# Kernel optimization log

Hardware: AMD Instinct MI355X
Metric: run time of the kernel (lower is better)

The kernel has to match this reference:

```python
import jax, jax.numpy as jnp
import numpy as np

D_MODEL, N_HEADS, D_K, D_FF, N_LAYERS, VOCAB, TGT_LEN = 512, 8, 64, 2048, 4, 32000, 1024
B, S_ENC = 4, 1024


def layernorm(x, g, b, eps=1e-6):
    mu = jnp.mean(x, axis=-1, keepdims=True)
    var = jnp.var(x, axis=-1, keepdims=True)
    return g * (x - mu) / jnp.sqrt(var + eps) + b


def sinusoid_pos_enc(seq_len, d_model):
    # source indexes positions 5 .. tgt_len+4 into the sinusoid table
    pos = jnp.arange(5, seq_len + 5, dtype=jnp.float32)[:, None]
    i = jnp.arange(d_model)
    angle = pos / jnp.power(10000.0, (2 * (i // 2)).astype(jnp.float32) / d_model)
    return jnp.where(i % 2 == 0, jnp.sin(angle), jnp.cos(angle))


def mha(xq, xkv, W, b, g, beta, mask):
    # W: [4, d, d] = (Wq, Wk, Wv, Wo); mask: [B,1,q,k], attend where mask != 0
    Bsz, Sq, _ = xq.shape
    q = (xq @ W[0] + b[0]).reshape(Bsz, Sq, N_HEADS, D_K).transpose(0, 2, 1, 3)
    k = (xkv @ W[1] + b[1]).reshape(Bsz, -1, N_HEADS, D_K).transpose(0, 2, 1, 3)
    v = (xkv @ W[2] + b[2]).reshape(Bsz, -1, N_HEADS, D_K).transpose(0, 2, 1, 3)
    scores = jnp.einsum('bhqd,bhkd->bhqk', q, k) / jnp.sqrt(jnp.float32(D_K))
    scores = jnp.where(mask == 0, jnp.float32(-1e9), scores)
    attn = jax.nn.softmax(scores, axis=-1)
    ctx = jnp.einsum('bhqk,bhkd->bhqd', attn, v).transpose(0, 2, 1, 3).reshape(Bsz, Sq, D_MODEL)
    out = ctx @ W[3] + b[3]
    return layernorm(out + xq, g, beta)


def setup_inputs() -> dict:
    key = jax.random.key(0)
    ks = jax.random.split(key, 8)
    sc = 0.02
    return {
        'dec_inputs': jax.random.randint(ks[0], (B, TGT_LEN), 0, VOCAB, dtype=jnp.int32),
        'enc_inputs': jax.random.randint(ks[1], (B, S_ENC), 0, 50, dtype=jnp.int32),
        'enc_outputs': jax.random.normal(ks[2], (B, S_ENC, D_MODEL), jnp.float32),
        'tgt_emb': jax.random.normal(ks[3], (VOCAB, D_MODEL), jnp.float32) * sc,
        'self_W': jax.random.normal(ks[4], (N_LAYERS, 4, D_MODEL, D_MODEL), jnp.float32) * sc,
        'self_b': jnp.zeros((N_LAYERS, 4, D_MODEL), jnp.float32),
        'enc_W': jax.random.normal(ks[5], (N_LAYERS, 4, D_MODEL, D_MODEL), jnp.float32) * sc,
        'enc_b': jnp.zeros((N_LAYERS, 4, D_MODEL), jnp.float32),
        'ffn_W1': jax.random.normal(ks[6], (N_LAYERS, D_MODEL, D_FF), jnp.float32) * sc,
        'ffn_b1': jnp.zeros((N_LAYERS, D_FF), jnp.float32),
        'ffn_W2': jax.random.normal(ks[7], (N_LAYERS, D_FF, D_MODEL), jnp.float32) * sc,
        'ffn_b2': jnp.zeros((N_LAYERS, D_MODEL), jnp.float32),
        'ln_g': jnp.ones((N_LAYERS, 3, D_MODEL), jnp.float32),
        'ln_b': jnp.zeros((N_LAYERS, 3, D_MODEL), jnp.float32),
    }


def reference(dec_inputs, enc_inputs, enc_outputs, tgt_emb, self_W, self_b, enc_W, enc_b,
              ffn_W1, ffn_b1, ffn_W2, ffn_b2, ln_g, ln_b):
    Bsz, S = dec_inputs.shape
    x = tgt_emb[dec_inputs] + sinusoid_pos_enc(S, D_MODEL)
    # self-attn mask: (pad_k OR lower-triangular) > 0, attend where nonzero (as in source)
    pad_self = (dec_inputs == 0).astype(jnp.float32)[:, None, None, :]      # [B,1,1,S]
    sub = jnp.tril(jnp.ones((S, S), jnp.float32))                           # [S,S]
    self_mask = ((pad_self + sub) > 0).astype(jnp.float32)                  # [B,1,S,S]
    # cross-attn mask: 1 where enc key is PAD; attend where nonzero (as in source)
    cross_mask = (enc_inputs == 0).astype(jnp.float32)[:, None, None, :]    # [B,1,1,S_enc]

    def step(h, p):
        sW, sb, eW, eb, W1, b1, W2, b2, g, bb = p
        h = mha(h, h, sW, sb, g[0], bb[0], self_mask)
        h = mha(h, enc_outputs, eW, eb, g[1], bb[1], cross_mask)
        f = jax.nn.relu(h @ W1 + b1) @ W2 + b2   # Conv1D(k=1) == pointwise dense
        h = layernorm(f + h, g[2], bb[2])
        return h, None

    x, _ = jax.lax.scan(step, x, (self_W, self_b, enc_W, enc_b,
                                  ffn_W1, ffn_b1, ffn_W2, ffn_b2, ln_g, ln_b))
    return x


if __name__ == '__main__':
    out = reference(**setup_inputs())
    print(out.shape, out.dtype)
```

## Files before the change

kernel.cpp:

```cpp
#include <hip/hip_runtime.h>
#include <math.h>

#define D_MODEL 512
#define N_HEADS 8
#define D_KH    64
#define D_FF    2048
#define N_LAYERS 4
#define BSZ     4
#define SEQ     1024

typedef __attribute__((ext_vector_type(8))) __bf16 bf16x8;
typedef __attribute__((ext_vector_type(8))) short  s16x8;
typedef __attribute__((ext_vector_type(4))) float  f32x4;

union BF8 { s16x8 s; bf16x8 b; };

static __device__ inline unsigned short f2b(float f) {
    unsigned u = __float_as_uint(f);
    unsigned r = (u + 0x7fffu + ((u >> 16) & 1u)) >> 16;
    return (unsigned short)r;
}

static __device__ __forceinline__ void async16(const unsigned short* g, unsigned short* l) {
    __builtin_amdgcn_global_load_lds((const __attribute__((address_space(1))) unsigned int*)g,
                                     (__attribute__((address_space(3))) unsigned int*)l, 16, 0, 0);
}

__global__ void embed_kernel(const int* __restrict__ dec, const float* __restrict__ emb,
                             float* __restrict__ x, unsigned short* __restrict__ xb) {
    int idx = blockIdx.x * blockDim.x + threadIdx.x;
    int d  = idx % D_MODEL;
    int bs = idx / D_MODEL;
    int s  = bs % SEQ;
    int tok = dec[bs];
    float pos = (float)(s + 5);
    float e = (float)(d & ~1) * (1.0f / (float)D_MODEL);
    float ang = pos * __expf(-9.210340372f * e);
    float pe = (d & 1) ? __cosf(ang) : __sinf(ang);
    float v = emb[(size_t)tok * D_MODEL + d] + pe;
    x[idx] = v;
    xb[idx] = f2b(v);
}

__global__ void cvt_bf16_kernel(const float* __restrict__ in, unsigned short* __restrict__ outp, int n4) {
    int i = blockIdx.x * blockDim.x + threadIdx.x;
    if (i < n4) {
        float4 f = ((const float4*)in)[i];
        ushort4 h;
        h.x = f2b(f.x); h.y = f2b(f.y); h.z = f2b(f.z); h.w = f2b(f.w);
        ((ushort4*)outp)[i] = h;
    }
}

__global__ void wt_all_kernel(const float* __restrict__ selfW, const float* __restrict__ encW,
                              const float* __restrict__ W1, const float* __restrict__ W2,
                              unsigned short* __restrict__ wtS, unsigned short* __restrict__ wtE,
                              unsigned short* __restrict__ wtF1, unsigned short* __restrict__ wtF2) {
    __shared__ unsigned short Tb[64][72];
    int tile = blockIdx.x;
    int which = tile >> 10, rem = tile & 1023;
    const float* src; unsigned short* dst; int K, N, z, kt, ntile;
    if (which <= 1) {
        src = which ? encW : selfW; dst = which ? wtE : wtS;
        K = 512; N = 512;
        z = rem >> 6; int r2 = rem & 63; kt = r2 & 7; ntile = r2 >> 3;
    } else if (which == 2) {
        src = W1; dst = wtF1; K = 512; N = 2048;
        z = rem >> 8; int r2 = rem & 255; kt = r2 & 7; ntile = r2 >> 3;
    } else {
        src = W2; dst = wtF2; K = 2048; N = 512;
        z = rem >> 8; int r2 = rem & 255; kt = r2 >> 3; ntile = r2 & 7;
    }
    int k0 = kt * 64, n0 = ntile * 64;
    size_t zoff = (size_t)z * K * N;
    src += zoff; dst += zoff;
    int t = threadIdx.x;
    int kr = t & 63, sg = t >> 6;
    const float* sp = src + (size_t)(k0 + kr) * N + n0 + sg * 16;
    #pragma unroll
    for (int j = 0; j < 4; j++) {
        float4 f = *(const float4*)(sp + 4 * j);
        Tb[sg * 16 + 4 * j + 0][kr] = f2b(f.x);
        Tb[sg * 16 + 4 * j + 1][kr] = f2b(f.y);
        Tb[sg * 16 + 4 * j + 2][kr] = f2b(f.z);
        Tb[sg * 16 + 4 * j + 3][kr] = f2b(f.w);
    }
    __syncthreads();
    unsigned short* dp = dst + (size_t)(n0 + kr) * K + k0 + sg * 16;
    *(s16x8*)(dp)     = *(const s16x8*)&Tb[kr][sg * 16];
    *(s16x8*)(dp + 8) = *(const s16x8*)&Tb[kr][sg * 16 + 8];
}

__global__ void prep_kernel(const int* __restrict__ dec, const int* __restrict__ enc,
                            int* __restrict__ cntEnc, int* __restrict__ listEnc,
                            int* __restrict__ anyPadDec) {
    int b = blockIdx.x;
    int lane = threadIdx.x;
    int base = 0;
    for (int c0 = 0; c0 < SEQ; c0 += 64) {
        bool z = (enc[b * SEQ + c0 + lane] == 0);
        unsigned long long mask = __ballot(z);
        int pre = __popcll(mask & ((1ull << lane) - 1ull));
        if (z) listEnc[b * SEQ + base + pre] = c0 + lane;
        base += __popcll(mask);
    }
    if (lane == 0) cntEnc[b] = base;
    for (int c0 = 0; c0 < SEQ; c0 += 64) {
        bool z = (dec[b * SEQ + c0 + lane] == 0);
        unsigned long long mask = __ballot(z);
        if (lane == 0) anyPadDec[b * (SEQ / 64) + (c0 >> 6)] = (mask != 0ull) ? 1 : 0;
    }
}

template<int OUTBF16, int RELU, int QKV>
__launch_bounds__(256, 3)
__global__ void gemm_lds_kernel(const unsigned short* __restrict__ A, const unsigned short* __restrict__ A1,
                                const unsigned short* __restrict__ Wt, const float* __restrict__ bias,
                                void* __restrict__ C_, void* __restrict__ C1, void* __restrict__ C2,
                                int M, int N, int K) {
    __shared__ unsigned short lds[2][12288];
    int m0 = blockIdx.x * 128, n0;
    if (QKV) {
        int j = blockIdx.y >> 3;
        n0 = (int)(blockIdx.y & 7) * 64;
        Wt += (size_t)j * (D_MODEL * D_MODEL);
        bias += j * D_MODEL;
        if (j) A = A1;
        if (j == 1) C_ = C1; else if (j == 2) C_ = C2;
    } else n0 = blockIdx.y * 64;

    int t = threadIdx.x, w = t >> 6, lane = t & 63;
    int g = lane >> 4, c = lane & 15;
    int l3 = lane >> 3, l7 = lane & 7;
    int srcoff = 8 * (l7 ^ l3);

    const unsigned short* Abase = A  + (size_t)m0 * K;
    const unsigned short* Bbase = Wt + (size_t)n0 * K;

    f32x4 acc[2][4];
    #pragma unroll
    for (int mi = 0; mi < 2; mi++)
        #pragma unroll
        for (int nj = 0; nj < 4; nj++) acc[mi][nj] = (f32x4){0.f, 0.f, 0.f, 0.f};

#define STAGE(BUF, KT) do {                                                         \
        unsigned short* Lb_ = &lds[BUF][0];                                         \
        int k0_ = (KT) * 64;                                                        \
        _Pragma("unroll")                                                           \
        for (int i_ = 0; i_ < 4; i_++) {                                            \
            int q_ = w * 4 + i_;                                                    \
            async16(Abase + (size_t)(q_ * 8 + l3) * K + k0_ + srcoff, Lb_ + q_ * 512); \
        }                                                                           \
        _Pragma("unroll")                                                           \
        for (int i_ = 0; i_ < 2; i_++) {                                            \
            int q_ = w * 2 + i_;                                                    \
            async16(Bbase + (size_t)(q_ * 8 + l3) * K + k0_ + srcoff, Lb_ + 8192 + q_ * 512); \
        }                                                                           \
    } while (0)

    int nt = K >> 6;
    STAGE(0, 0);
    __syncthreads();
    for (int kt = 0; kt < nt; kt++) {
        int cur = kt & 1;
        if (kt + 1 < nt) STAGE(cur ^ 1, kt + 1);
        const unsigned short* Lb = &lds[cur][0];
        BF8 a[2][2], b[2][4];
        #pragma unroll
        for (int kk = 0; kk < 2; kk++) {
            int xo = (kk * 32 + g * 8) ^ ((c & 7) * 8);
            #pragma unroll
            for (int mi = 0; mi < 2; mi++)
                a[kk][mi].s = *(const s16x8*)&Lb[(w * 32 + mi * 16 + c) * 64 + xo];
            #pragma unroll
            for (int nj = 0; nj < 4; nj++)
                b[kk][nj].s = *(const s16x8*)&Lb[8192 + (nj * 16 + c) * 64 + xo];
        }
        #pragma unroll
        for (int kk = 0; kk < 2; kk++)
            #pragma unroll
            for (int mi = 0; mi < 2; mi++)
                #pragma unroll
                for (int nj = 0; nj < 4; nj++)
                    acc[mi][nj] = __builtin_amdgcn_mfma_f32_16x16x32_bf16(a[kk][mi].b, b[kk][nj].b, acc[mi][nj], 0, 0, 0);
        __syncthreads();
    }
#undef STAGE

    #pragma unroll
    for (int mi = 0; mi < 2; mi++) {
        #pragma unroll
        for (int nj = 0; nj < 4; nj++) {
            #pragma unroll
            for (int r = 0; r < 4; r++) {
                int row = m0 + w * 32 + mi * 16 + g * 4 + r;
                int col = n0 + nj * 16 + c;
                float v = acc[mi][nj][r] + bias[col];
                if (RELU) v = fmaxf(v, 0.0f);
                if (OUTBF16) ((unsigned short*)C_)[(size_t)row * N + col] = f2b(v);
                else         ((float*)C_)[(size_t)row * N + col] = v;
            }
        }
    }
}

template<int OUTBF16, int RELU>
__launch_bounds__(256, 4)
__global__ void gemm64_kernel(const unsigned short* __restrict__ A,
                              const unsigned short* __restrict__ Wt, const float* __restrict__ bias,
                              void* __restrict__ C_, int M, int N, int K) {
    __shared__ unsigned short lds[2][8192];
    int m0 = blockIdx.x * 64, n0 = blockIdx.y * 64;

    int t = threadIdx.x, w = t >> 6, lane = t & 63;
    int wm = w >> 1, wn = w & 1;
    int g = lane >> 4, c = lane & 15;
    int l3 = lane >> 3, l7 = lane & 7;
    int srcoff = 8 * (l7 ^ l3);

    const unsigned short* Abase = A  + (size_t)m0 * K;
    const unsigned short* Bbase = Wt + (size_t)n0 * K;

    f32x4 acc[2][2];
    #pragma unroll
    for (int mi = 0; mi < 2; mi++)
        #pragma unroll
        for (int nj = 0; nj < 2; nj++) acc[mi][nj] = (f32x4){0.f, 0.f, 0.f, 0.f};

#define STAGE64(BUF, KT) do {                                                       \
        unsigned short* Lb_ = &lds[BUF][0];                                         \
        int k0_ = (KT) * 64;                                                        \
        _Pragma("unroll")                                                           \
        for (int i_ = 0; i_ < 2; i_++) {                                            \
            int q_ = w * 2 + i_;                                                    \
            async16(Abase + (size_t)(q_ * 8 + l3) * K + k0_ + srcoff, Lb_ + q_ * 512); \
            async16(Bbase + (size_t)(q_ * 8 + l3) * K + k0_ + srcoff, Lb_ + 4096 + q_ * 512); \
        }                                                                           \
    } while (0)

    int nt = K >> 6;
    STAGE64(0, 0);
    __syncthreads();
    for (int kt = 0; kt < nt; kt++) {
        int cur = kt & 1;
        if (kt + 1 < nt) STAGE64(cur ^ 1, kt + 1);
        const unsigned short* Lb = &lds[cur][0];
        BF8 a[2][2], b[2][2];
        #pragma unroll
        for (int kk = 0; kk < 2; kk++) {
            int xo = (kk * 32 + g * 8) ^ ((c & 7) * 8);
            #pragma unroll
            for (int mi = 0; mi < 2; mi++)
                a[kk][mi].s = *(const s16x8*)&Lb[(wm * 32 + mi * 16 + c) * 64 + xo];
            #pragma unroll
            for (int nj = 0; nj < 2; nj++)
                b[kk][nj].s = *(const s16x8*)&Lb[4096 + (wn * 32 + nj * 16 + c) * 64 + xo];
        }
        #pragma unroll
        for (int kk = 0; kk < 2; kk++)
            #pragma unroll
            for (int mi = 0; mi < 2; mi++)
                #pragma unroll
                for (int nj = 0; nj < 2; nj++)
                    acc[mi][nj] = __builtin_amdgcn_mfma_f32_16x16x32_bf16(a[kk][mi].b, b[kk][nj].b, acc[mi][nj], 0, 0, 0);
        __syncthreads();
    }
#undef STAGE64

    #pragma unroll
    for (int mi = 0; mi < 2; mi++) {
        #pragma unroll
        for (int nj = 0; nj < 2; nj++) {
            #pragma unroll
            for (int r = 0; r < 4; r++) {
                int row = m0 + wm * 32 + mi * 16 + g * 4 + r;
                int col = n0 + wn * 32 + nj * 16 + c;
                float v = acc[mi][nj][r] + bias[col];
                if (RELU) v = fmaxf(v, 0.0f);
                if (OUTBF16) ((unsigned short*)C_)[(size_t)row * N + col] = f2b(v);
                else         ((float*)C_)[(size_t)row * N + col] = v;
            }
        }
    }
}

template<int OUTBF16, int RELU>
__launch_bounds__(256, 2)
__global__ void gemm128_kernel(const unsigned short* __restrict__ A,
                               const unsigned short* __restrict__ Wt, const float* __restrict__ bias,
                               void* __restrict__ C_, int M, int N, int K) {
    __shared__ unsigned short lds[2][16384];
    int m0 = blockIdx.x * 128, n0 = blockIdx.y * 128;

    int t = threadIdx.x, w = t >> 6, lane = t & 63;
    int wm = w >> 1, wn = w & 1;
    int g = lane >> 4, c = lane & 15;
    int l3 = lane >> 3, l7 = lane & 7;
    int srcoff = 8 * (l7 ^ l3);

    const unsigned short* Abase = A  + (size_t)m0 * K;
    const unsigned short* Bbase = Wt + (size_t)n0 * K;

    f32x4 acc[4][4];
    #pragma unroll
    for (int mi = 0; mi < 4; mi++)
        #pragma unroll
        for (int nj = 0; nj < 4; nj++) acc[mi][nj] = (f32x4){0.f, 0.f, 0.f, 0.f};

#define STAGE128(BUF, KT) do {                                                      \
        unsigned short* Lb_ = &lds[BUF][0];                                         \
        int k0_ = (KT) * 64;                                                        \
        _Pragma("unroll")                                                           \
        for (int i_ = 0; i_ < 4; i_++) {                                            \
            int q_ = w * 4 + i_;                                                    \
            async16(Abase + (size_t)(q_ * 8 + l3) * K + k0_ + srcoff, Lb_ + q_ * 512); \
            async16(Bbase + (size_t)(q_ * 8 + l3) * K + k0_ + srcoff, Lb_ + 8192 + q_ * 512); \
        }                                                                           \
    } while (0)

    int nt = K >> 6;
    STAGE128(0, 0);
    __syncthreads();
    for (int kt = 0; kt < nt; kt++) {
        int cur = kt & 1;
        if (kt + 1 < nt) STAGE128(cur ^ 1, kt + 1);
        const unsigned short* Lb = &lds[cur][0];
        BF8 a[2][4], b[2][4];
        #pragma unroll
        for (int kk = 0; kk < 2; kk++) {
            int xo = (kk * 32 + g * 8) ^ ((c & 7) * 8);
            #pragma unroll
            for (int mi = 0; mi < 4; mi++)
                a[kk][mi].s = *(const s16x8*)&Lb[(wm * 64 + mi * 16 + c) * 64 + xo];
            #pragma unroll
            for (int nj = 0; nj < 4; nj++)
                b[kk][nj].s = *(const s16x8*)&Lb[8192 + (wn * 64 + nj * 16 + c) * 64 + xo];
        }
        #pragma unroll
        for (int kk = 0; kk < 2; kk++)
            #pragma unroll
            for (int mi = 0; mi < 4; mi++)
                #pragma unroll
                for (int nj = 0; nj < 4; nj++)
                    acc[mi][nj] = __builtin_amdgcn_mfma_f32_16x16x32_bf16(a[kk][mi].b, b[kk][nj].b, acc[mi][nj], 0, 0, 0);
        __syncthreads();
    }
#undef STAGE128

    #pragma unroll
    for (int mi = 0; mi < 4; mi++) {
        #pragma unroll
        for (int nj = 0; nj < 4; nj++) {
            #pragma unroll
            for (int r = 0; r < 4; r++) {
                int row = m0 + wm * 64 + mi * 16 + g * 4 + r;
                int col = n0 + wn * 64 + nj * 16 + c;
                float v = acc[mi][nj][r] + bias[col];
                if (RELU) v = fmaxf(v, 0.0f);
                if (OUTBF16) ((unsigned short*)C_)[(size_t)row * N + col] = f2b(v);
                else         ((float*)C_)[(size_t)row * N + col] = v;
            }
        }
    }
}

#define RS 72
template<int MODE>
__global__ void attn_kernel(const unsigned short* __restrict__ Q, const unsigned short* __restrict__ K,
                            const unsigned short* __restrict__ V, const int* __restrict__ ids,
                            const int* __restrict__ list, const int* __restrict__ cnt,
                            const int* __restrict__ anyPad,
                            unsigned short* __restrict__ O_, int Sq, int Sk) {
    __shared__ unsigned short Kl[2][64][RS];
    __shared__ unsigned short Vt[2][64][RS];
    __shared__ unsigned short Ps[4][16][RS];
    __shared__ short act[16];
    __shared__ int nActS;

    int blk = blockIdx.x;
    int qt, bh;
    if (MODE) {
        int hi = blk >> 8, pair = blk & 255;
        bh = pair >> 3;
        int qtp = pair & 7;
        qt = hi ? (15 - qtp) : qtp;
    } else {
        qt = blk & 15;
        bh = blk >> 4;
    }
    int h = bh % N_HEADS;
    int b = bh / N_HEADS;
    int qbase = qt * 64;
    int t = threadIdx.x;
    int w = t >> 6, lane = t & 63;
    int g = lane >> 4, c = lane & 15;

    BF8 qf[2];
    {
        int qrow = qbase + w * 16 + c;
        const unsigned short* qp = Q + ((size_t)(b * Sq + qrow)) * D_MODEL + h * D_KH;
        qf[0].s = *(const s16x8*)(qp + 8 * g);
        qf[1].s = *(const s16x8*)(qp + 8 * g + 32);
    }

    int nk = 0;
    bool gathered = false;
    if (!MODE) {
        nk = cnt[b];
        gathered = (nk > 0);
    }

    if (t == 0) {
        int n = 0;
        if (MODE) {
            for (int kt2 = 0; kt2 < (Sk >> 6); kt2++)
                if (kt2 <= qt || anyPad[b * (Sk >> 6) + kt2]) act[n++] = (short)kt2;
        } else {
            int tt = gathered ? ((nk + 63) >> 6) : (Sk >> 6);
            for (int kt2 = 0; kt2 < tt; kt2++) act[n++] = (short)kt2;
        }
        nActS = n;
    }
    __syncthreads();
    int nAct = nActS;

    float m[4], l[4];
    f32x4 Oacc[4];
    #pragma unroll
    for (int r = 0; r < 4; r++) { m[r] = -INFINITY; l[r] = 0.0f; }
    #pragma unroll
    for (int ds = 0; ds < 4; ds++) Oacc[ds] = (f32x4){0.f, 0.f, 0.f, 0.f};

    s16x8 kreg0, kreg1, vreg0, vreg1;
    int kr0 = t >> 3,        ks0 = t & 7;
    int kr1 = (t + 256) >> 3, ks1 = (t + 256) & 7;

#define LOADT(KT) do {                                                                \
        int k0_ = (KT) * 64;                                                          \
        int krow0 = k0_ + kr0, krow1 = k0_ + kr1;                                     \
        if (gathered) {                                                               \
            krow0 = list[b * Sk + (krow0 < nk ? krow0 : nk - 1)];                     \
            krow1 = list[b * Sk + (krow1 < nk ? krow1 : nk - 1)];                     \
        }                                                                             \
        kreg0 = *(const s16x8*)(K + ((size_t)(b * Sk + krow0)) * D_MODEL + h * D_KH + ks0 * 8); \
        kreg1 = *(const s16x8*)(K + ((size_t)(b * Sk + krow1)) * D_MODEL + h * D_KH + ks1 * 8); \
        int li = k0_ + lane, vrow = li;                                               \
        if (gathered) vrow = list[b * Sk + (li < nk ? li : nk - 1)];                  \
        const unsigned short* vp = V + ((size_t)(b * Sk + vrow)) * D_MODEL + h * D_KH + w * 16; \
        vreg0 = *(const s16x8*)(vp);                                                  \
        vreg1 = *(const s16x8*)(vp + 8);                                              \
    } while (0)

#define WRITET(BUF) do {                                                              \
        *(s16x8*)&Kl[BUF][kr0][ks0 * 8] = kreg0;                                      \
        *(s16x8*)&Kl[BUF][kr1][ks1 * 8] = kreg1;                                      \
        _Pragma("unroll")                                                             \
        for (int j = 0; j < 8; j++) Vt[BUF][w * 16 + j][lane] = ((unsigned short*)&vreg0)[j]; \
        _Pragma("unroll")                                                             \
        for (int j = 0; j < 8; j++) Vt[BUF][w * 16 + 8 + j][lane] = ((unsigned short*)&vreg1)[j]; \
    } while (0)

    LOADT(act[0]);
    WRITET(0);
    __syncthreads();
    for (int i = 0; i < nAct; i++) {
        int cur = i & 1;
        int k0 = (int)act[i] * 64;
        if (i + 1 < nAct) LOADT(act[i + 1]);

        f32x4 S[4];
        #pragma unroll
        for (int sub = 0; sub < 4; sub++) {
            BF8 b0, b1;
            b0.s = *(const s16x8*)&Kl[cur][sub * 16 + c][8 * g];
            b1.s = *(const s16x8*)&Kl[cur][sub * 16 + c][8 * g + 32];
            f32x4 s = (f32x4){0.f, 0.f, 0.f, 0.f};
            s = __builtin_amdgcn_mfma_f32_16x16x32_bf16(qf[0].b, b0.b, s, 0, 0, 0);
            s = __builtin_amdgcn_mfma_f32_16x16x32_bf16(qf[1].b, b1.b, s, 0, 0, 0);
            S[sub] = s;
        }

        #pragma unroll
        for (int sub = 0; sub < 4; sub++) {
            int k = k0 + sub * 16 + c;
            bool pad;
            if (MODE) pad = (ids[b * Sk + k] == 0);
            else      pad = gathered ? (k < nk) : false;
            #pragma unroll
            for (int r = 0; r < 4; r++) {
                bool att;
                if (MODE) {
                    int qrow = qbase + w * 16 + g * 4 + r;
                    att = pad || (k <= qrow);
                } else att = pad;
                S[sub][r] = att ? S[sub][r] * 0.125f : -1e9f;
            }
        }

        #pragma unroll
        for (int r = 0; r < 4; r++) {
            float mx = fmaxf(fmaxf(S[0][r], S[1][r]), fmaxf(S[2][r], S[3][r]));
            #pragma unroll
            for (int o = 8; o > 0; o >>= 1) mx = fmaxf(mx, __shfl_xor(mx, o));
            float mn = fmaxf(m[r], mx);
            float sc = __expf(m[r] - mn);
            float lsum = 0.f;
            #pragma unroll
            for (int sub = 0; sub < 4; sub++) {
                float p = __expf(S[sub][r] - mn);
                S[sub][r] = p;
                lsum += p;
            }
            #pragma unroll
            for (int o = 8; o > 0; o >>= 1) lsum += __shfl_xor(lsum, o);
            l[r] = l[r] * sc + lsum;
            m[r] = mn;
            #pragma unroll
            for (int ds = 0; ds < 4; ds++) Oacc[ds][r] *= sc;
        }

        #pragma unroll
        for (int sub = 0; sub < 4; sub++)
            #pragma unroll
            for (int r = 0; r < 4; r++)
                Ps[w][g * 4 + r][sub * 16 + c] = f2b(S[sub][r]);

        #pragma unroll
        for (int kk = 0; kk < 2; kk++) {
            BF8 pa;
            pa.s = *(const s16x8*)&Ps[w][c][8 * g + kk * 32];
            #pragma unroll
            for (int ds = 0; ds < 4; ds++) {
                BF8 vb;
                vb.s = *(const s16x8*)&Vt[cur][ds * 16 + c][8 * g + kk * 32];
                Oacc[ds] = __builtin_amdgcn_mfma_f32_16x16x32_bf16(pa.b, vb.b, Oacc[ds], 0, 0, 0);
            }
        }

        if (i + 1 < nAct) WRITET(cur ^ 1);
        __syncthreads();
    }
#undef LOADT
#undef WRITET

    #pragma unroll
    for (int r = 0; r < 4; r++) {
        float inv = 1.0f / l[r];
        int qrow = qbase + w * 16 + g * 4 + r;
        unsigned short* op = O_ + ((size_t)(b * Sq + qrow)) * D_MODEL + h * D_KH;
        #pragma unroll
        for (int ds = 0; ds < 4; ds++)
            op[ds * 16 + c] = f2b(Oacc[ds][r] * inv);
    }
}

template<int WRITEB>
__global__ void ln_residual_kernel(const float* __restrict__ f, const float* __restrict__ h,
                                   const float* __restrict__ g, const float* __restrict__ bb,
                                   float* __restrict__ out, unsigned short* __restrict__ outb) {
    int row  = blockIdx.x * 4 + threadIdx.x / 64;
    int lane = threadIdx.x % 64;
    const float* fr = f + (size_t)row * D_MODEL;
    const float* hr = h + (size_t)row * D_MODEL;
    float v[8];
    float s = 0.f;
    #pragma unroll
    for (int i = 0; i < 8; i++) {
        v[i] = fr[lane + i * 64] + hr[lane + i * 64];
        s += v[i];
    }
    #pragma unroll
    for (int o = 32; o > 0; o >>= 1) s += __shfl_xor(s, o);
    float mu = s * (1.0f / 512.0f);
    float ss = 0.f;
    #pragma unroll
    for (int i = 0; i < 8; i++) { float d = v[i] - mu; ss += d * d; }
    #pragma unroll
    for (int o = 32; o > 0; o >>= 1) ss += __shfl_xor(ss, o);
    float var = ss * (1.0f / 512.0f);
    float inv = 1.0f / sqrtf(var + 1e-6f);
    #pragma unroll
    for (int i = 0; i < 8; i++) {
        int d = lane + i * 64;
        float o2 = g[d] * (v[i] - mu) * inv + bb[d];
        out[(size_t)row * D_MODEL + d] = o2;
        if (WRITEB) outb[(size_t)row * D_MODEL + d] = f2b(o2);
    }
}

extern "C" void kernel_launch(void* const* d_in, const int* in_sizes, int n_in,
                              void* d_out, int out_size, void* d_ws, size_t ws_size,
                              hipStream_t stream) {
    const int*   dec     = (const int*)d_in[0];
    const int*   enc_ids = (const int*)d_in[1];
    const float* enc_out = (const float*)d_in[2];
    const float* emb     = (const float*)d_in[3];
    const float* self_W  = (const float*)d_in[4];
    const float* self_b  = (const float*)d_in[5];
    const float* enc_W   = (const float*)d_in[6];
    const float* enc_b   = (const float*)d_in[7];
    const float* W1      = (const float*)d_in[8];
    const float* b1      = (const float*)d_in[9];
    const float* W2      = (const float*)d_in[10];
    const float* b2      = (const float*)d_in[11];
    const float* ln_g    = (const float*)d_in[12];
    const float* ln_b    = (const float*)d_in[13];
    float* out = (float*)d_out;

    const size_t NTOK = (size_t)BSZ * SEQ;
    float* x  = (float*)d_ws;
    float* bA = x + NTOK * D_MODEL;
    unsigned short* xb   = (unsigned short*)(bA + NTOK * D_MODEL);
    unsigned short* encb = xb + NTOK * D_MODEL;
    unsigned short* bQ = encb + NTOK * D_MODEL;
    unsigned short* bK = bQ + NTOK * D_MODEL;
    unsigned short* bV = bK + NTOK * D_MODEL;
    unsigned short* bD = bV + NTOK * D_MODEL;
    unsigned short* bH = bQ;
    unsigned short* wtS  = bD + NTOK * D_MODEL;
    unsigned short* wtE  = wtS + (size_t)N_LAYERS * 4 * D_MODEL * D_MODEL;
    unsigned short* wtF1 = wtE + (size_t)N_LAYERS * 4 * D_MODEL * D_MODEL;
    unsigned short* wtF2 = wtF1 + (size_t)N_LAYERS * D_MODEL * D_FF;
    int* cntEnc    = (int*)(wtF2 + (size_t)N_LAYERS * D_FF * D_MODEL);
    int* anyPadDec = cntEnc + BSZ;
    int* listEnc   = anyPadDec + BSZ * (SEQ / 64);

    dim3 blk(256);
    embed_kernel<<<dim3((unsigned)(NTOK * D_MODEL / 256)), blk, 0, stream>>>(dec, emb, x, xb);
    cvt_bf16_kernel<<<dim3((unsigned)(NTOK * D_MODEL / 4 / 256)), blk, 0, stream>>>(enc_out, encb, (int)(NTOK * D_MODEL / 4));
    prep_kernel<<<dim3(BSZ), dim3(64), 0, stream>>>(dec, enc_ids, cntEnc, listEnc, anyPadDec);
    wt_all_kernel<<<dim3(4096), blk, 0, stream>>>(self_W, enc_W, W1, W2, wtS, wtE, wtF1, wtF2);

    int M = (int)NTOK;
    dim3 gqkv(M / 128, 24);
    dim3 gp64(M / 64, D_MODEL / 64);
    dim3 gf1 (M / 128, D_FF / 128);
    dim3 gf2 (M / 64, D_MODEL / 64);
    int nAttnBlk = BSZ * N_HEADS * (SEQ / 64);

    const size_t WT = (size_t)D_MODEL * D_MODEL;
    for (int L = 0; L < N_LAYERS; L++) {
        const unsigned short* sWt = wtS + (size_t)L * 4 * WT;
        const unsigned short* eWt = wtE + (size_t)L * 4 * WT;
        const float* sb = self_b + (size_t)L * 4 * D_MODEL;
        const float* eb = enc_b  + (size_t)L * 4 * D_MODEL;
        const float* g  = ln_g   + (size_t)L * 3 * D_MODEL;
        const float* bs = ln_b   + (size_t)L * 3 * D_MODEL;

        gemm_lds_kernel<1,0,1><<<gqkv, blk, 0, stream>>>(xb, xb, sWt, sb, bQ, bK, bV, M, D_MODEL, D_MODEL);
        attn_kernel<1><<<dim3(nAttnBlk), blk, 0, stream>>>(bQ, bK, bV, dec, listEnc, cntEnc, anyPadDec, bD, SEQ, SEQ);
        gemm64_kernel<0,0><<<gp64, blk, 0, stream>>>(bD, sWt + 3 * WT, sb + 3 * D_MODEL, bA, M, D_MODEL, D_MODEL);
        ln_residual_kernel<1><<<dim3(M / 4), blk, 0, stream>>>(bA, x, g + 0 * D_MODEL, bs + 0 * D_MODEL, x, xb);

        gemm_lds_kernel<1,0,1><<<gqkv, blk, 0, stream>>>(xb, encb, eWt, eb, bQ, bK, bV, M, D_MODEL, D_MODEL);
        attn_kernel<0><<<dim3(nAttnBlk), blk, 0, stream>>>(bQ, bK, bV, enc_ids, listEnc, cntEnc, anyPadDec, bD, SEQ, SEQ);
        gemm64_kernel<0,0><<<gp64, blk, 0, stream>>>(bD, eWt + 3 * WT, eb + 3 * D_MODEL, bA, M, D_MODEL, D_MODEL);
        ln_residual_kernel<1><<<dim3(M / 4), blk, 0, stream>>>(bA, x, g + 1 * D_MODEL, bs + 1 * D_MODEL, x, xb);

        gemm128_kernel<1,1><<<gf1, blk, 0, stream>>>(xb, wtF1 + (size_t)L * D_MODEL * D_FF, b1 + (size_t)L * D_FF,    bH, M, D_FF,    D_MODEL);
        gemm64_kernel<0,0><<<gf2, blk, 0, stream>>>(bH, wtF2 + (size_t)L * D_FF * D_MODEL, b2 + (size_t)L * D_MODEL, bA, M, D_MODEL, D_FF);
        float* lnout = (L == N_LAYERS - 1) ? out : x;
        ln_residual_kernel<1><<<dim3(M / 4), blk, 0, stream>>>(bA, x, g + 2 * D_MODEL, bs + 2 * D_MODEL, lnout, xb);
    }
}
```

Measured before the change: 570.8 us.

## Precompute cross-attention K/V for all layers in one batched GEMM

Cross-attention K and V depend only on the encoder outputs, so all four layers' K/V projections are computed up front in a single batched 64x64-tile GEMM launch with grid z over layer and K/V. Each layer's cross QKV launch becomes a Q-only projection. The one large launch gives better occupancy than many small ones. The embedding and encoder bf16 conversion kernels are also fused into one launch. This costs extra workspace for eight bf16 K/V buffers and adds a large kernel to the prologue.

```diff
diff --git a/kernel.cpp b/kernel.cpp
--- a/kernel.cpp
+++ b/kernel.cpp
@@ -26,29 +26,31 @@
                                      (__attribute__((address_space(3))) unsigned int*)l, 16, 0, 0);
 }
 
-__global__ void embed_kernel(const int* __restrict__ dec, const float* __restrict__ emb,
-                             float* __restrict__ x, unsigned short* __restrict__ xb) {
+__global__ void embed_cvt_kernel(const int* __restrict__ dec, const float* __restrict__ emb,
+                                 float* __restrict__ x, unsigned short* __restrict__ xb,
+                                 const float* __restrict__ enc_out, unsigned short* __restrict__ encb) {
+    const int NE = BSZ * SEQ * D_MODEL;
     int idx = blockIdx.x * blockDim.x + threadIdx.x;
-    int d  = idx % D_MODEL;
-    int bs = idx / D_MODEL;
-    int s  = bs % SEQ;
-    int tok = dec[bs];
-    float pos = (float)(s + 5);
-    float e = (float)(d & ~1) * (1.0f / (float)D_MODEL);
-    float ang = pos * __expf(-9.210340372f * e);
-    float pe = (d & 1) ? __cosf(ang) : __sinf(ang);
-    float v = emb[(size_t)tok * D_MODEL + d] + pe;
-    x[idx] = v;
-    xb[idx] = f2b(v);
-}
-
-__global__ void cvt_bf16_kernel(const float* __restrict__ in, unsigned short* __restrict__ outp, int n4) {
-    int i = blockIdx.x * blockDim.x + threadIdx.x;
-    if (i < n4) {
-        float4 f = ((const float4*)in)[i];
-        ushort4 h;
-        h.x = f2b(f.x); h.y = f2b(f.y); h.z = f2b(f.z); h.w = f2b(f.w);
-        ((ushort4*)outp)[i] = h;
+    if (idx < NE) {
+        int d  = idx % D_MODEL;
+        int bs = idx / D_MODEL;
+        int s  = bs % SEQ;
+        int tok = dec[bs];
+        float pos = (float)(s + 5);
+        float e = (float)(d & ~1) * (1.0f / (float)D_MODEL);
+        float ang = pos * __expf(-9.210340372f * e);
+        float pe = (d & 1) ? __cosf(ang) : __sinf(ang);
+        float v = emb[(size_t)tok * D_MODEL + d] + pe;
+        x[idx] = v;
+        xb[idx] = f2b(v);
+    } else {
+        int i = idx - NE;
+        if (i < NE / 4) {
+            float4 f = ((const float4*)enc_out)[i];
+            ushort4 h;
+            h.x = f2b(f.x); h.y = f2b(f.y); h.z = f2b(f.z); h.w = f2b(f.w);
+            ((ushort4*)encb)[i] = h;
+        }
     }
 }
 
@@ -284,6 +286,87 @@
     }
 }
 
+__launch_bounds__(256, 4)
+__global__ void gemm_kv_kernel(const unsigned short* __restrict__ A,
+                               const unsigned short* __restrict__ wtE, const float* __restrict__ enc_b,
+                               unsigned short* __restrict__ outKV) {
+    __shared__ unsigned short lds[2][8192];
+    const int K = D_MODEL, N = D_MODEL;
+    int j = blockIdx.z, L = j >> 1, kv = j & 1;
+    const unsigned short* Wt = wtE + ((size_t)L * 4 + 1 + kv) * (D_MODEL * D_MODEL);
+    const float* bias = enc_b + (L * 4 + 1 + kv) * D_MODEL;
+    unsigned short* C_ = outKV + (size_t)j * (BSZ * SEQ) * D_MODEL;
+
+    int m0 = blockIdx.x * 64, n0 = blockIdx.y * 64;
+    int t = threadIdx.x, w = t >> 6, lane = t & 63;
+    int wm = w >> 1, wn = w & 1;
+    int g = lane >> 4, c = lane & 15;
+    int l3 = lane >> 3, l7 = lane & 7;
+    int srcoff = 8 * (l7 ^ l3);
+
+    const unsigned short* Abase = A  + (size_t)m0 * K;
+    const unsigned short* Bbase = Wt + (size_t)n0 * K;
+
+    f32x4 acc[2][2];
+    #pragma unroll
+    for (int mi = 0; mi < 2; mi++)
+        #pragma unroll
+        for (int nj = 0; nj < 2; nj++) acc[mi][nj] = (f32x4){0.f, 0.f, 0.f, 0.f};
+
+#define STAGEKV(BUF, KT) do {                                                       \
+        unsigned short* Lb_ = &lds[BUF][0];                                         \
+        int k0_ = (KT) * 64;                                                        \
+        _Pragma("unroll")                                                           \
+        for (int i_ = 0; i_ < 2; i_++) {                                            \
+            int q_ = w * 2 + i_;                                                    \
+            async16(Abase + (size_t)(q_ * 8 + l3) * K + k0_ + srcoff, Lb_ + q_ * 512); \
+            async16(Bbase + (size_t)(q_ * 8 + l3) * K + k0_ + srcoff, Lb_ + 4096 + q_ * 512); \
+        }                                                                           \
+    } while (0)
+
+    int nt = K >> 6;
+    STAGEKV(0, 0);
+    __syncthreads();
+    for (int kt = 0; kt < nt; kt++) {
+        int cur = kt & 1;
+        if (kt + 1 < nt) STAGEKV(cur ^ 1, kt + 1);
+        const unsigned short* Lb = &lds[cur][0];
+        BF8 a[2][2], b[2][2];
+        #pragma unroll
+        for (int kk = 0; kk < 2; kk++) {
+            int xo = (kk * 32 + g * 8) ^ ((c & 7) * 8);
+            #pragma unroll
+            for (int mi = 0; mi < 2; mi++)
+                a[kk][mi].s = *(const s16x8*)&Lb[(wm * 32 + mi * 16 + c) * 64 + xo];
+            #pragma unroll
+            for (int nj = 0; nj < 2; nj++)
+                b[kk][nj].s = *(const s16x8*)&Lb[4096 + (wn * 32 + nj * 16 + c) * 64 + xo];
+        }
+        #pragma unroll
+        for (int kk = 0; kk < 2; kk++)
+            #pragma unroll
+            for (int mi = 0; mi < 2; mi++)
+                #pragma unroll
+                for (int nj = 0; nj < 2; nj++)
+                    acc[mi][nj] = __builtin_amdgcn_mfma_f32_16x16x32_bf16(a[kk][mi].b, b[kk][nj].b, acc[mi][nj], 0, 0, 0);
+        __syncthreads();
+    }
+#undef STAGEKV
+
+    #pragma unroll
+    for (int mi = 0; mi < 2; mi++) {
+        #pragma unroll
+        for (int nj = 0; nj < 2; nj++) {
+            #pragma unroll
+            for (int r = 0; r < 4; r++) {
+                int row = m0 + wm * 32 + mi * 16 + g * 4 + r;
+                int col = n0 + wn * 32 + nj * 16 + c;
+                C_[(size_t)row * N + col] = f2b(acc[mi][nj][r] + bias[col]);
+            }
+        }
+    }
+}
+
 template<int OUTBF16, int RELU>
 __launch_bounds__(256, 2)
 __global__ void gemm128_kernel(const unsigned short* __restrict__ A,
@@ -621,15 +704,20 @@
     unsigned short* wtE  = wtS + (size_t)N_LAYERS * 4 * D_MODEL * D_MODEL;
     unsigned short* wtF1 = wtE + (size_t)N_LAYERS * 4 * D_MODEL * D_MODEL;
     unsigned short* wtF2 = wtF1 + (size_t)N_LAYERS * D_MODEL * D_FF;
-    int* cntEnc    = (int*)(wtF2 + (size_t)N_LAYERS * D_FF * D_MODEL);
+    unsigned short* crossKV = wtF2 + (size_t)N_LAYERS * D_FF * D_MODEL;
+    int* cntEnc    = (int*)(crossKV + (size_t)8 * NTOK * D_MODEL);
     int* anyPadDec = cntEnc + BSZ;
     int* listEnc   = anyPadDec + BSZ * (SEQ / 64);
 
     dim3 blk(256);
-    embed_kernel<<<dim3((unsigned)(NTOK * D_MODEL / 256)), blk, 0, stream>>>(dec, emb, x, xb);
-    cvt_bf16_kernel<<<dim3((unsigned)(NTOK * D_MODEL / 4 / 256)), blk, 0, stream>>>(enc_out, encb, (int)(NTOK * D_MODEL / 4));
+    {
+        const int NE = (int)(NTOK * D_MODEL);
+        int total = NE + NE / 4;
+        embed_cvt_kernel<<<dim3((total + 255) / 256), blk, 0, stream>>>(dec, emb, x, xb, enc_out, encb);
+    }
     prep_kernel<<<dim3(BSZ), dim3(64), 0, stream>>>(dec, enc_ids, cntEnc, listEnc, anyPadDec);
     wt_all_kernel<<<dim3(4096), blk, 0, stream>>>(self_W, enc_W, W1, W2, wtS, wtE, wtF1, wtF2);
+    gemm_kv_kernel<<<dim3((unsigned)(NTOK / 64), D_MODEL / 64, 8), blk, 0, stream>>>(encb, wtE, enc_b, crossKV);
 
     int M = (int)NTOK;
     dim3 gqkv(M / 128, 24);
@@ -646,14 +734,16 @@
         const float* eb = enc_b  + (size_t)L * 4 * D_MODEL;
         const float* g  = ln_g   + (size_t)L * 3 * D_MODEL;
         const float* bs = ln_b   + (size_t)L * 3 * D_MODEL;
+        const unsigned short* bKc = crossKV + (size_t)(L * 2 + 0) * NTOK * D_MODEL;
+        const unsigned short* bVc = crossKV + (size_t)(L * 2 + 1) * NTOK * D_MODEL;
 
         gemm_lds_kernel<1,0,1><<<gqkv, blk, 0, stream>>>(xb, xb, sWt, sb, bQ, bK, bV, M, D_MODEL, D_MODEL);
         attn_kernel<1><<<dim3(nAttnBlk), blk, 0, stream>>>(bQ, bK, bV, dec, listEnc, cntEnc, anyPadDec, bD, SEQ, SEQ);
         gemm64_kernel<0,0><<<gp64, blk, 0, stream>>>(bD, sWt + 3 * WT, sb + 3 * D_MODEL, bA, M, D_MODEL, D_MODEL);
         ln_residual_kernel<1><<<dim3(M / 4), blk, 0, stream>>>(bA, x, g + 0 * D_MODEL, bs + 0 * D_MODEL, x, xb);
 
-        gemm_lds_kernel<1,0,1><<<gqkv, blk, 0, stream>>>(xb, encb, eWt, eb, bQ, bK, bV, M, D_MODEL, D_MODEL);
-        attn_kernel<0><<<dim3(nAttnBlk), blk, 0, stream>>>(bQ, bK, bV, enc_ids, listEnc, cntEnc, anyPadDec, bD, SEQ, SEQ);
+        gemm64_kernel<1,0><<<gp64, blk, 0, stream>>>(xb, eWt + 0 * WT, eb + 0 * D_MODEL, bQ, M, D_MODEL, D_MODEL);
+        attn_kernel<0><<<dim3(nAttnBlk), blk, 0, stream>>>(bQ, bKc, bVc, enc_ids, listEnc, cntEnc, anyPadDec, bD, SEQ, SEQ);
         gemm64_kernel<0,0><<<gp64, blk, 0, stream>>>(bD, eWt + 3 * WT, eb + 3 * D_MODEL, bA, M, D_MODEL, D_MODEL);
         ln_residual_kernel<1><<<dim3(M / 4), blk, 0, stream>>>(bA, x, g + 1 * D_MODEL, bs + 1 * D_MODEL, x, xb);
 
```

New measurement: 575.1 us. About the same (+0.8%).
